# Kernel optimization log

Measured on AMD Instinct MI355X. Metric: run time of the kernel, lower is better.

The kernel has to match this reference:

```python
import jax, jax.numpy as jnp
import numpy as np

EMBED_DIM = 768
NUM_HEADS = 12


def setup_inputs() -> dict:
    key = jax.random.key(0)
    ks = jax.random.split(key, 9)
    B, N, C = 16, 1024, EMBED_DIM
    std = 1.0 / np.sqrt(C)
    x = jax.random.normal(ks[0], (B, N, C), dtype=jnp.float32)
    def w(k):
        return jax.random.normal(k, (C, C), dtype=jnp.float32) * std
    def b(k):
        return jax.random.normal(k, (C,), dtype=jnp.float32) * 0.01
    return {
        "x": x,
        "Wq": w(ks[1]), "bq": b(ks[2]),
        "Wk": w(ks[3]), "bk": b(ks[4]),
        "Wv": w(ks[5]), "bv": b(ks[6]),
        "Wo": w(ks[7]), "bo": b(ks[8]),
    }


def reference(x, Wq, bq, Wk, bk, Wv, bv, Wo, bo):
    B, N, C = x.shape
    H = NUM_HEADS
    Dh = C // H
    scale = 1.0 / np.sqrt(Dh)

    q = x @ Wq + bq  # (B, N, C)
    k = x @ Wk + bk
    v = x @ Wv + bv

    # Faithful to the original: (B, N, H, Dh) -> reshape(B*H, N, Dh)
    # WITHOUT transposing, exactly as torch_mla_core does (row-major reshape).
    q2 = q.reshape(B * H, N, Dh)
    k2 = k.reshape(B * H, N, Dh)
    v2 = v.reshape(B * H, N, Dh)

    scores = jnp.einsum('gld,gmd->glm', q2, k2) * scale  # (B*H, N, N)
    attn = jax.nn.softmax(scores, axis=-1)
    ctx2 = jnp.einsum('glm,gmd->gld', attn, v2)  # (B*H, N, Dh)

    ctx = ctx2.reshape(B, H, N, Dh).transpose(0, 2, 1, 3).reshape(B, N, C)
    out = ctx @ Wo + bo
    return out
```

## Files before the change

### kernel.cpp

```cpp
#include <hip/hip_runtime.h>
#include <hip/hip_bf16.h>
#include <cstdint>
#include <cstddef>

typedef unsigned short u16;
typedef __attribute__((ext_vector_type(8))) short s8v;
typedef __attribute__((ext_vector_type(4))) float f4v;
typedef __attribute__((ext_vector_type(8))) u16 u16x8;
typedef __attribute__((ext_vector_type(4))) uint32_t u32x4;

#define AS1 __attribute__((address_space(1)))
#define AS3 __attribute__((address_space(3)))

#define BATCH 16
#define SEQ   1024
#define EMBED 768
#define HEADS 12
#define DH    64
#define MTOT  (BATCH*SEQ)

__device__ __forceinline__ u16 f2bf(float f) {
    union { float f; uint32_t u; } v; v.f = f;
    uint32_t r = v.u + 0x7fffu + ((v.u >> 16) & 1u);
    return (u16)(r >> 16);
}

__device__ __forceinline__ void gll16(const u16* g, u16* l) {
    __builtin_amdgcn_global_load_lds((AS1 void*)g, (AS3 void*)l, 16, 0, 0);
}

#define XBLOCKS 12288
#define TBLOCKS 576
__global__ void k_pack(const float* __restrict__ x, u16* __restrict__ xb, int nx,
                       const float* __restrict__ Wq, const float* __restrict__ Wk,
                       const float* __restrict__ Wv, const float* __restrict__ Wo,
                       const float* __restrict__ bq, const float* __restrict__ bk,
                       const float* __restrict__ bv,
                       u16* __restrict__ wqkvT, u16* __restrict__ woT,
                       float* __restrict__ bqkv)
{
    __shared__ __attribute__((aligned(16))) u16 ts[64 * 80];
    const int tid = threadIdx.x;
    if (blockIdx.x < XBLOCKS) {
        int i = (blockIdx.x * 256 + tid) * 4;
        if (i + 3 < nx) {
            float4 f = *(const float4*)(x + i);
            ushort4 o;
            o.x = f2bf(f.x); o.y = f2bf(f.y); o.z = f2bf(f.z); o.w = f2bf(f.w);
            *(ushort4*)(xb + i) = o;
        }
        return;
    }
    int tb = blockIdx.x - XBLOCKS;
    if (tb < TBLOCKS) {
        const float* src; u16* dst; int n0, k0, nn0; float sc;
        if (tb < 432) {
            int nt = tb % 36, kt = tb / 36;
            n0 = nt * 64; k0 = kt * 64; dst = wqkvT;
            if (n0 < 768)       { src = Wq; nn0 = n0;        sc = 0.125f; }
            else if (n0 < 1536) { src = Wk; nn0 = n0 - 768;  sc = 1.0f;   }
            else                { src = Wv; nn0 = n0 - 1536; sc = 1.0f;   }
        } else {
            int tb2 = tb - 432;
            int nt = tb2 % 12, kt = tb2 / 12;
            n0 = nt * 64; k0 = kt * 64; nn0 = n0; sc = 1.0f;
            src = Wo; dst = woT;
        }
        const int r = tid >> 2, cb = (tid & 3) * 16;
#pragma unroll
        for (int i = 0; i < 4; ++i) {
            float4 f = *(const float4*)(src + (size_t)(k0 + r) * 768 + nn0 + cb + i * 4);
            ts[(cb + i * 4 + 0) * 80 + r] = f2bf(f.x * sc);
            ts[(cb + i * 4 + 1) * 80 + r] = f2bf(f.y * sc);
            ts[(cb + i * 4 + 2) * 80 + r] = f2bf(f.z * sc);
            ts[(cb + i * 4 + 3) * 80 + r] = f2bf(f.w * sc);
        }
        __syncthreads();
#pragma unroll
        for (int j = 0; j < 2; ++j) {
            u16x8 tv = *(const u16x8*)(ts + r * 80 + cb + j * 8);
            *(u16x8*)(dst + (size_t)(n0 + r) * 768 + k0 + cb + j * 8) = tv;
        }
        return;
    }
    int t3 = (tb - TBLOCKS) * 256 + tid;
    if (t3 < 2304) {
        bqkv[t3] = (t3 < 768) ? bq[t3] * 0.125f
                 : ((t3 < 1536) ? bk[t3 - 768] : bv[t3 - 1536]);
    }
}

template<int MODE>
__global__ __launch_bounds__(256) void k_gemm(
    const u16* __restrict__ A, const u16* __restrict__ BT,
    const float* __restrict__ bias,
    u16* __restrict__ oq, u16* __restrict__ okk, u16* __restrict__ ov,
    float* __restrict__ of)
{
    __shared__ __attribute__((aligned(16))) u16 As[128 * 32];
    __shared__ __attribute__((aligned(16))) u16 Bs[128 * 32];
    const int tid = threadIdx.x;
    const int m0 = blockIdx.x * 128;
    const int n0 = blockIdx.y * 128;
    const int wv = tid >> 6;
    const int ln = tid & 63;
    const int l15 = ln & 15, quad = ln >> 4;
    const int wm = (wv >> 1) * 64, wn = (wv & 1) * 64;
    const int r = tid >> 2, c8 = (tid & 3) * 8;

    const u16* gA0 = A + (size_t)(m0 + r) * 768 + c8;
    const u16* gA1 = gA0 + 64 * 768;
    const u16* gB0 = BT + (size_t)(n0 + r) * 768 + c8;
    const u16* gB1 = gB0 + 64 * 768;
    u16* lA0 = As + wv * 512;
    u16* lA1 = As + 2048 + wv * 512;
    u16* lB0 = Bs + wv * 512;
    u16* lB1 = Bs + 2048 + wv * 512;

    f4v acc[4][4] = {};

    for (int kt = 0; kt < 24; ++kt) {
        const int ko = kt * 32;
        gll16(gA0 + ko, lA0);
        gll16(gA1 + ko, lA1);
        gll16(gB0 + ko, lB0);
        gll16(gB1 + ko, lB1);
        __syncthreads();
        s8v aF[4], bF[4];
#pragma unroll
        for (int i = 0; i < 4; ++i)
            aF[i] = *(const s8v*)(As + (wm + i * 16 + l15) * 32 + quad * 8);
#pragma unroll
        for (int j = 0; j < 4; ++j)
            bF[j] = *(const s8v*)(Bs + (wn + j * 16 + l15) * 32 + quad * 8);
#pragma unroll
        for (int i = 0; i < 4; ++i)
#pragma unroll
            for (int j = 0; j < 4; ++j)
                acc[i][j] = __builtin_amdgcn_mfma_f32_16x16x32_bf16(aF[i], bF[j], acc[i][j], 0, 0, 0);
        __syncthreads();
    }

#pragma unroll
    for (int j = 0; j < 4; ++j) {
        int n = n0 + wn + j * 16 + l15;
        float bs = bias[n];
        if (MODE == 0) {
            u16* dst; int nn;
            if (n < 768)       { dst = oq;  nn = n; }
            else if (n < 1536) { dst = okk; nn = n - 768; }
            else               { dst = ov;  nn = n - 1536; }
#pragma unroll
            for (int i = 0; i < 4; ++i) {
                int mrow = m0 + wm + i * 16 + quad * 4;
#pragma unroll
                for (int rg = 0; rg < 4; ++rg)
                    dst[(size_t)(mrow + rg) * 768 + nn] = f2bf(acc[i][j][rg] + bs);
            }
        } else {
#pragma unroll
            for (int i = 0; i < 4; ++i) {
                int mrow = m0 + wm + i * 16 + quad * 4;
#pragma unroll
                for (int rg = 0; rg < 4; ++rg)
                    of[(size_t)(mrow + rg) * 768 + n] = acc[i][j][rg] + bs;
            }
        }
    }
}

__global__ void k_transpose_v(const u16* __restrict__ v, u16* __restrict__ vt) {
    __shared__ __attribute__((aligned(16))) u16 ts[64 * 80];
    int g = blockIdx.x >> 4;
    int l0 = (blockIdx.x & 15) << 6;
    const u16* vg = v + (size_t)g * 65536;
    u16* vtg = vt + (size_t)g * 65536;
    int tid = threadIdx.x;
#pragma unroll
    for (int c = tid; c < 512; c += 256) {
        int l = c >> 3, d0 = (c & 7) * 8;
        *(uint4*)(ts + l * 80 + d0) = *(const uint4*)(vg + (size_t)(l0 + l) * 64 + d0);
    }
    __syncthreads();
#pragma unroll
    for (int c = tid; c < 512; c += 256) {
        int d = c >> 3, lc = (c & 7) * 8;
        u16x8 tv;
#pragma unroll
        for (int i = 0; i < 8; ++i) tv[i] = ts[(lc + i) * 80 + d];
        *(u16x8*)(vtg + (size_t)d * 1024 + l0 + lc) = tv;
    }
}

#define KS2(r_, c_) ( ((r_) << 6) + (((((c_) >> 3) ^ ((r_) & 7)) & 7) << 3) + ((c_) & 7) )

__global__ __launch_bounds__(256) void k_attn(
    const u16* __restrict__ qb, const u16* __restrict__ kb,
    const u16* __restrict__ vt, u16* __restrict__ ctx)
{
    __shared__ __attribute__((aligned(16))) u16 Ks[128 * 64];
    __shared__ __attribute__((aligned(16))) u16 Vts[64 * 136];

    const int g = blockIdx.x >> 3;
    const int q0 = (blockIdx.x & 7) << 7;
    const int tid = threadIdx.x, wv = tid >> 6;
    const int ln = tid & 63, l15 = ln & 15, quad = ln >> 4;
    const u16* qg = qb + (size_t)g * 65536;
    const u16* kg = kb + (size_t)g * 65536;
    const u16* vtg = vt + (size_t)g * 65536;

    const int krr = tid >> 3, kcb = (tid & 7) * 8;
    const int vd = tid >> 4, vc0 = (tid & 15) * 8;
    const u16* kgp = kg + (size_t)krr * 64 + kcb;
    const u16* vgp = vtg + (size_t)vd * 1024 + vc0;

    uint4 kr0 = *(const uint4*)(kgp);
    uint4 kr1 = *(const uint4*)(kgp + 2048);
    uint4 kr2 = *(const uint4*)(kgp + 4096);
    uint4 kr3 = *(const uint4*)(kgp + 6144);
    uint4 vr0 = *(const uint4*)(vgp);
    uint4 vr1 = *(const uint4*)(vgp + 16384);
    uint4 vr2 = *(const uint4*)(vgp + 32768);
    uint4 vr3 = *(const uint4*)(vgp + 49152);

    const u16* qrow = qg + (size_t)(q0 + wv * 32 + l15) * 64 + quad * 8;
    s8v aQ00 = *(const s8v*)qrow;
    s8v aQ01 = *(const s8v*)(qrow + 32);
    s8v aQ10 = *(const s8v*)(qrow + 1024);
    s8v aQ11 = *(const s8v*)(qrow + 1024 + 32);

    f4v o0[4] = {}, o1[4] = {};
    float rsum0 = 0.f, rsum1 = 0.f;

    for (int jt = 0; jt < 8; ++jt) {
        __builtin_amdgcn_s_barrier();
        __builtin_amdgcn_sched_barrier(0);

        *(uint4*)(Ks + KS2(krr,      kcb)) = kr0;
        *(uint4*)(Ks + KS2(krr + 32, kcb)) = kr1;
        *(uint4*)(Ks + KS2(krr + 64, kcb)) = kr2;
        *(uint4*)(Ks + KS2(krr + 96, kcb)) = kr3;
        *(uint4*)(Vts + (vd     ) * 136 + vc0) = vr0;
        *(uint4*)(Vts + (vd + 16) * 136 + vc0) = vr1;
        *(uint4*)(Vts + (vd + 32) * 136 + vc0) = vr2;
        *(uint4*)(Vts + (vd + 48) * 136 + vc0) = vr3;

        if (jt < 7) {
            const size_t koff = (size_t)(jt + 1) * 8192;
            const int voff = (jt + 1) * 128;
            kr0 = *(const uint4*)(kgp + koff);
            kr1 = *(const uint4*)(kgp + koff + 2048);
            kr2 = *(const uint4*)(kgp + koff + 4096);
            kr3 = *(const uint4*)(kgp + koff + 6144);
            vr0 = *(const uint4*)(vgp + voff);
            vr1 = *(const uint4*)(vgp + voff + 16384);
            vr2 = *(const uint4*)(vgp + voff + 32768);
            vr3 = *(const uint4*)(vgp + voff + 49152);
        }

        asm volatile("s_waitcnt lgkmcnt(0)" ::: "memory");
        __builtin_amdgcn_s_barrier();
        __builtin_amdgcn_sched_barrier(0);

        f4v s0[8], s1[8];
        __builtin_amdgcn_s_setprio(1);
#pragma unroll
        for (int ns = 0; ns < 8; ++ns) {
            int rK = ns * 16 + l15;
            s8v b0 = *(const s8v*)(Ks + KS2(rK, quad * 8));
            s8v b1 = *(const s8v*)(Ks + KS2(rK, quad * 8 + 32));
            f4v t0 = {};
            t0 = __builtin_amdgcn_mfma_f32_16x16x32_bf16(b0, aQ00, t0, 0, 0, 0);
            t0 = __builtin_amdgcn_mfma_f32_16x16x32_bf16(b1, aQ01, t0, 0, 0, 0);
            s0[ns] = t0;
            f4v t1 = {};
            t1 = __builtin_amdgcn_mfma_f32_16x16x32_bf16(b0, aQ10, t1, 0, 0, 0);
            t1 = __builtin_amdgcn_mfma_f32_16x16x32_bf16(b1, aQ11, t1, 0, 0, 0);
            s1[ns] = t1;
        }
        __builtin_amdgcn_s_setprio(0);

        s8v aP0[4], aP1[4];
#pragma unroll
        for (int ns = 0; ns < 8; ++ns)
#pragma unroll
            for (int rg = 0; rg < 4; ++rg) {
                float p = __expf(s0[ns][rg]);
                s0[ns][rg] = p;
                rsum0 += p;
            }
#pragma unroll
        for (int ks = 0; ks < 4; ++ks) {
            uint32_t a0, a1, c0, c1;
            asm("v_cvt_pk_bf16_f32 %0, %1, %2" : "=v"(a0) : "v"(s0[2*ks][0]),   "v"(s0[2*ks][1]));
            asm("v_cvt_pk_bf16_f32 %0, %1, %2" : "=v"(a1) : "v"(s0[2*ks][2]),   "v"(s0[2*ks][3]));
            asm("v_cvt_pk_bf16_f32 %0, %1, %2" : "=v"(c0) : "v"(s0[2*ks+1][0]), "v"(s0[2*ks+1][1]));
            asm("v_cvt_pk_bf16_f32 %0, %1, %2" : "=v"(c1) : "v"(s0[2*ks+1][2]), "v"(s0[2*ks+1][3]));
            asm("v_permlane32_swap_b32 %0, %1" : "+v"(a0), "+v"(c0));
            asm("v_permlane16_swap_b32 %0, %1" : "+v"(a0), "+v"(c0));
            asm("v_permlane32_swap_b32 %0, %1" : "+v"(a1), "+v"(c1));
            asm("v_permlane16_swap_b32 %0, %1" : "+v"(a1), "+v"(c1));
            u32x4 pk; pk.x = a0; pk.y = a1; pk.z = c0; pk.w = c1;
            aP0[ks] = __builtin_bit_cast(s8v, pk);
        }
#pragma unroll
        for (int ns = 0; ns < 8; ++ns)
#pragma unroll
            for (int rg = 0; rg < 4; ++rg) {
                float p = __expf(s1[ns][rg]);
                s1[ns][rg] = p;
                rsum1 += p;
            }
#pragma unroll
        for (int ks = 0; ks < 4; ++ks) {
            uint32_t a0, a1, c0, c1;
            asm("v_cvt_pk_bf16_f32 %0, %1, %2" : "=v"(a0) : "v"(s1[2*ks][0]),   "v"(s1[2*ks][1]));
            asm("v_cvt_pk_bf16_f32 %0, %1, %2" : "=v"(a1) : "v"(s1[2*ks][2]),   "v"(s1[2*ks][3]));
            asm("v_cvt_pk_bf16_f32 %0, %1, %2" : "=v"(c0) : "v"(s1[2*ks+1][0]), "v"(s1[2*ks+1][1]));
            asm("v_cvt_pk_bf16_f32 %0, %1, %2" : "=v"(c1) : "v"(s1[2*ks+1][2]), "v"(s1[2*ks+1][3]));
            asm("v_permlane32_swap_b32 %0, %1" : "+v"(a0), "+v"(c0));
            asm("v_permlane16_swap_b32 %0, %1" : "+v"(a0), "+v"(c0));
            asm("v_permlane32_swap_b32 %0, %1" : "+v"(a1), "+v"(c1));
            asm("v_permlane16_swap_b32 %0, %1" : "+v"(a1), "+v"(c1));
            u32x4 pk; pk.x = a0; pk.y = a1; pk.z = c0; pk.w = c1;
            aP1[ks] = __builtin_bit_cast(s8v, pk);
        }

        __builtin_amdgcn_s_setprio(1);
#pragma unroll
        for (int ks = 0; ks < 4; ++ks)
#pragma unroll
            for (int ds = 0; ds < 4; ++ds) {
                s8v bV = *(const s8v*)(Vts + (ds * 16 + l15) * 136 + ks * 32 + quad * 8);
                o0[ds] = __builtin_amdgcn_mfma_f32_16x16x32_bf16(aP0[ks], bV, o0[ds], 0, 0, 0);
                o1[ds] = __builtin_amdgcn_mfma_f32_16x16x32_bf16(aP1[ks], bV, o1[ds], 0, 0, 0);
            }
        __builtin_amdgcn_s_setprio(0);
    }

    rsum0 += __shfl_xor(rsum0, 16, 64);
    rsum0 += __shfl_xor(rsum0, 32, 64);
    rsum1 += __shfl_xor(rsum1, 16, 64);
    rsum1 += __shfl_xor(rsum1, 32, 64);

    const int b = g / 12, h = g % 12;
    u16* cbase = ctx + (size_t)b * 786432 + h * 64;
#pragma unroll
    for (int rg = 0; rg < 4; ++rg) {
        int row0 = q0 + wv * 32 + quad * 4 + rg;
        float inv0 = 1.0f / __shfl(rsum0, 20 * quad + rg, 64);
#pragma unroll
        for (int ds = 0; ds < 4; ++ds)
            cbase[(size_t)row0 * 768 + ds * 16 + l15] = f2bf(o0[ds][rg] * inv0);
        int row1 = row0 + 16;
        float inv1 = 1.0f / __shfl(rsum1, 20 * quad + rg, 64);
#pragma unroll
        for (int ds = 0; ds < 4; ++ds)
            cbase[(size_t)row1 * 768 + ds * 16 + l15] = f2bf(o1[ds][rg] * inv1);
    }
}

extern "C" void kernel_launch(void* const* d_in, const int* in_sizes, int n_in,
                              void* d_out, int out_size, void* d_ws, size_t ws_size,
                              hipStream_t stream) {
    const float* x  = (const float*)d_in[0];
    const float* Wq = (const float*)d_in[1];
    const float* bq = (const float*)d_in[2];
    const float* Wk = (const float*)d_in[3];
    const float* bk = (const float*)d_in[4];
    const float* Wv = (const float*)d_in[5];
    const float* bv = (const float*)d_in[6];
    const float* Wo = (const float*)d_in[7];
    const float* bo = (const float*)d_in[8];
    float* out = (float*)d_out;

    const size_t NTOK = (size_t)MTOT * EMBED;
    char* w = (char*)d_ws;
    u16* xb    = (u16*)w;              w += NTOK * 2;
    u16* qb    = (u16*)w;              w += NTOK * 2;
    u16* kb    = (u16*)w;              w += NTOK * 2;
    u16* vb    = (u16*)w;              w += NTOK * 2;
    u16* vtb   = (u16*)w;              w += NTOK * 2;
    u16* wqkvT = (u16*)w;              w += (size_t)2304 * 768 * 2;
    u16* woT   = (u16*)w;              w += (size_t)768 * 768 * 2;
    float* bqkv = (float*)w;           w += 2304 * 4;
    u16* ctx = xb;

    k_pack<<<XBLOCKS + TBLOCKS + 9, 256, 0, stream>>>(x, xb, (int)NTOK,
        Wq, Wk, Wv, Wo, bq, bk, bv, wqkvT, woT, bqkv);

    dim3 g1(128, 18);
    k_gemm<0><<<g1, 256, 0, stream>>>(xb, wqkvT, bqkv, qb, kb, vb, nullptr);

    k_transpose_v<<<3072, 256, 0, stream>>>(vb, vtb);
    k_attn<<<1536, 256, 0, stream>>>(qb, kb, vtb, ctx);

    dim3 g2(128, 6);
    k_gemm<1><<<g2, 256, 0, stream>>>(ctx, woT, bo, nullptr, nullptr, nullptr, out);
}
```

Measured before the change: 321.8 us.

## Double GEMM K-tile to 64 and XOR-swizzle LDS layout

The projection GEMM kernel now loads 64-wide K slices per iteration instead of 32, halving the number of loop iterations and barrier pairs. It also applies an XOR swizzle on the 16-byte chunk index within each LDS row, used both when writing via global-to-LDS loads and when reading MFMA fragments, to avoid bank conflicts. The cost is doubled LDS use per block (32 KB), which may reduce occupancy.

Result: slower. 329.3 us (+2.3%).

```diff
diff --git a/kernel.cpp b/kernel.cpp
--- a/kernel.cpp
+++ b/kernel.cpp
@@ -97,8 +97,8 @@
     u16* __restrict__ oq, u16* __restrict__ okk, u16* __restrict__ ov,
     float* __restrict__ of)
 {
-    __shared__ __attribute__((aligned(16))) u16 As[128 * 32];
-    __shared__ __attribute__((aligned(16))) u16 Bs[128 * 32];
+    __shared__ __attribute__((aligned(16))) u16 As[128 * 64];
+    __shared__ __attribute__((aligned(16))) u16 Bs[128 * 64];
     const int tid = threadIdx.x;
     const int m0 = blockIdx.x * 128;
     const int n0 = blockIdx.y * 128;
@@ -106,38 +106,46 @@
     const int ln = tid & 63;
     const int l15 = ln & 15, quad = ln >> 4;
     const int wm = (wv >> 1) * 64, wn = (wv & 1) * 64;
-    const int r = tid >> 2, c8 = (tid & 3) * 8;
-
-    const u16* gA0 = A + (size_t)(m0 + r) * 768 + c8;
-    const u16* gA1 = gA0 + 64 * 768;
-    const u16* gB0 = BT + (size_t)(n0 + r) * 768 + c8;
-    const u16* gB1 = gB0 + 64 * 768;
-    u16* lA0 = As + wv * 512;
-    u16* lA1 = As + 2048 + wv * 512;
-    u16* lB0 = Bs + wv * 512;
-    u16* lB1 = Bs + 2048 + wv * 512;
+
+    const int srow = tid >> 3;
+    const int schnk = ((tid & 7) ^ (srow & 7)) * 8;
+    const u16* gA = A + (size_t)(m0 + srow) * 768 + schnk;
+    const u16* gB = BT + (size_t)(n0 + srow) * 768 + schnk;
+    u16* lA = As + wv * 512;
+    u16* lB = Bs + wv * 512;
+
+    const int sl0 = ((quad)     ^ (l15 & 7)) * 8;
+    const int sl1 = ((4 + quad) ^ (l15 & 7)) * 8;
 
     f4v acc[4][4] = {};
 
-    for (int kt = 0; kt < 24; ++kt) {
-        const int ko = kt * 32;
-        gll16(gA0 + ko, lA0);
-        gll16(gA1 + ko, lA1);
-        gll16(gB0 + ko, lB0);
-        gll16(gB1 + ko, lB1);
+    for (int kt = 0; kt < 12; ++kt) {
+        const int ko = kt * 64;
+#pragma unroll
+        for (int i = 0; i < 4; ++i) {
+            gll16(gA + (size_t)i * 32 * 768 + ko, lA + i * 2048);
+            gll16(gB + (size_t)i * 32 * 768 + ko, lB + i * 2048);
+        }
         __syncthreads();
-        s8v aF[4], bF[4];
-#pragma unroll
-        for (int i = 0; i < 4; ++i)
-            aF[i] = *(const s8v*)(As + (wm + i * 16 + l15) * 32 + quad * 8);
-#pragma unroll
-        for (int j = 0; j < 4; ++j)
-            bF[j] = *(const s8v*)(Bs + (wn + j * 16 + l15) * 32 + quad * 8);
-#pragma unroll
-        for (int i = 0; i < 4; ++i)
-#pragma unroll
-            for (int j = 0; j < 4; ++j)
-                acc[i][j] = __builtin_amdgcn_mfma_f32_16x16x32_bf16(aF[i], bF[j], acc[i][j], 0, 0, 0);
+
+        s8v aF[4][2];
+#pragma unroll
+        for (int i = 0; i < 4; ++i) {
+            const u16* base = As + (wm + i * 16 + l15) * 64;
+            aF[i][0] = *(const s8v*)(base + sl0);
+            aF[i][1] = *(const s8v*)(base + sl1);
+        }
+#pragma unroll
+        for (int j = 0; j < 4; ++j) {
+            const u16* base = Bs + (wn + j * 16 + l15) * 64;
+            s8v bF0 = *(const s8v*)(base + sl0);
+            s8v bF1 = *(const s8v*)(base + sl1);
+#pragma unroll
+            for (int i = 0; i < 4; ++i) {
+                acc[i][j] = __builtin_amdgcn_mfma_f32_16x16x32_bf16(aF[i][0], bF0, acc[i][j], 0, 0, 0);
+                acc[i][j] = __builtin_amdgcn_mfma_f32_16x16x32_bf16(aF[i][1], bF1, acc[i][j], 0, 0, 0);
+            }
+        }
         __syncthreads();
     }
 
```
